# Kernel optimization log

Hardware: AMD Instinct MI355X
Metric: run time of the kernel (lower is better)

## Reference

```python
import jax, jax.numpy as jnp
import numpy as np

B, T, V, D, U = 256, 1024, 6, 64, 64  # batch, seq, vocab, embed dim, lstm units


def _lstm_dir(x_seq, mask_seq, Wk, Wr, b, reverse):
    # x_seq: [B,T,D], mask_seq: [B,T] bool. Keras gate order: i, f, g(cell), o.
    Bc, Tc, _ = x_seq.shape
    Uc = Wr.shape[0]
    if reverse:
        x_seq = x_seq[:, ::-1, :]
        mask_seq = mask_seq[:, ::-1]
    # precompute input projections for all timesteps (one big GEMM)
    xproj = jnp.einsum('btd,dg->tbg', x_seq, Wk) + b          # [T,B,4U]
    m = jnp.swapaxes(mask_seq, 0, 1)[..., None]               # [T,B,1]

    def step(carry, inp):
        h, c = carry
        xp, mt = inp
        z = xp + h @ Wr                                        # [B,4U]
        i, f, g, o = jnp.split(z, 4, axis=-1)
        i = jax.nn.sigmoid(i)
        f = jax.nn.sigmoid(f)
        g = jnp.tanh(g)
        o = jax.nn.sigmoid(o)
        c_new = f * c + i * g
        h_new = o * jnp.tanh(c_new)
        # masked steps carry state through and repeat previous output
        h = jnp.where(mt, h_new, h)
        c = jnp.where(mt, c_new, c)
        return (h, c), h

    h0 = jnp.zeros((Bc, Uc), x_seq.dtype)
    _, ys = jax.lax.scan(step, (h0, h0), (xproj, m))           # ys: [T,B,U]
    ys = jnp.swapaxes(ys, 0, 1)                                # [B,T,U]
    if reverse:
        ys = ys[:, ::-1, :]
    return ys


def reference(tokens, emb, Wk_f, Wr_f, b_f, Wk_b, Wr_b, b_b, Wd, bd):
    x = emb[tokens]                                            # [B,T,D]
    mask = jnp.any(x != 0, axis=-1)                            # Masking(0): all-zero feature vec -> masked
    y_f = _lstm_dir(x, mask, Wk_f, Wr_f, b_f, reverse=False)   # [B,T,U]
    y_b = _lstm_dir(x, mask, Wk_b, Wr_b, b_b, reverse=True)    # [B,T,U]
    y = jnp.concatenate([y_f, y_b], axis=-1)                   # [B,T,2U]
    last = y[:, -1, :]                                         # [B,2U]
    return last @ Wd + bd                                      # [B,1]


def setup_inputs() -> dict:
    key = jax.random.key(0)
    ks = jax.random.split(key, 8)
    return {
        'tokens': jax.random.randint(ks[0], (B, T), 0, V, dtype=jnp.int32),
        'emb': jax.random.normal(ks[1], (V, D), dtype=jnp.float32),
        'Wk_f': jax.random.normal(ks[2], (D, 4 * U), dtype=jnp.float32) * 0.05,
        'Wr_f': jax.random.normal(ks[3], (U, 4 * U), dtype=jnp.float32) * 0.05,
        'b_f': jnp.zeros((4 * U,), dtype=jnp.float32),
        'Wk_b': jax.random.normal(ks[4], (D, 4 * U), dtype=jnp.float32) * 0.05,
        'Wr_b': jax.random.normal(ks[5], (U, 4 * U), dtype=jnp.float32) * 0.05,
        'b_b': jnp.zeros((4 * U,), dtype=jnp.float32),
        'Wd': jax.random.normal(ks[6], (2 * U, 1), dtype=jnp.float32) * 0.05,
        'bd': jnp.zeros((1,), dtype=jnp.float32),
    }
```

## Files before the change

kernel.cpp:

```cpp
#include <hip/hip_runtime.h>


constexpr int kB = 256;
constexpr int kT = 1024;
constexpr int kV = 6;
constexpr int kD = 64;
constexpr int kU = 64;
constexpr int kG = 256;

#define LOG2E 1.44269504f

typedef _Float16 v2h __attribute__((ext_vector_type(2)));

template <int CTRL>
__device__ __forceinline__ float dppf(float x) {
    return __int_as_float(
        __builtin_amdgcn_mov_dpp(__float_as_int(x), CTRL, 0xF, 0xF, true));
}
constexpr int kBc0 = 0x00, kBc1 = 0x55, kBc2 = 0xAA, kBc3 = 0xFF;

__device__ __forceinline__ float fast_rcp(float x) { return __builtin_amdgcn_rcpf(x); }
__device__ __forceinline__ float exp2_f(float x)   { return __builtin_amdgcn_exp2f(x); }
__device__ __forceinline__ float sig_f(float z)  { return fast_rcp(1.0f + exp2_f(-LOG2E * z)); }
__device__ __forceinline__ float tanh_f(float z) { return 2.0f * fast_rcp(1.0f + exp2_f(-2.0f * LOG2E * z)) - 1.0f; }

__device__ __forceinline__ v2h as_v2h(float x) { return __builtin_bit_cast(v2h, x); }

__global__ __launch_bounds__(256)
__attribute__((amdgpu_waves_per_eu(1, 1)))
void bilstm_last_kernel(
    const int*   __restrict__ tokens,
    const float* __restrict__ emb,
    const float* __restrict__ Wk_f,
    const float* __restrict__ Wr_f,
    const float* __restrict__ b_f,
    const float* __restrict__ Wk_b,
    const float* __restrict__ b_b,
    const float* __restrict__ Wd,
    const float* __restrict__ bd,
    float*       __restrict__ out)
{
    __shared__ float s_emb[kV * kD];
    __shared__ float __align__(16) s_projP[kV * kG];
    __shared__ int   __align__(16) s_tok[kT];
    __shared__ _Float16 __align__(16) s_hh[2][kU];
    __shared__ float s_red[4];

    const int b   = blockIdx.x;
    const int tid = threadIdx.x;
    const int l   = tid & 63;
    const int wv  = tid >> 6;
    const int s   = l & 3;
    const int k   = l >> 2;
    const int u   = wv * 16 + k;
    const int col = s * kU + u;

    for (int i = tid; i < kV * kD; i += 256) s_emb[i] = emb[i];
    ((int4*)s_tok)[tid] = ((const int4*)(tokens + b * kT))[tid];
    if (tid < 2 * kU) ((_Float16*)s_hh)[tid] = (_Float16)0.f;
    __syncthreads();

    unsigned int mbv = 0;
#pragma unroll
    for (int v = 0; v < kV; ++v) {
        const unsigned long long bb = __ballot(s_emb[v * kD + l] != 0.0f);
        mbv |= (bb != 0ull) ? (1u << v) : 0u;
    }
    const unsigned int smb = __builtin_amdgcn_readfirstlane(mbv);

    const int tokL = __builtin_amdgcn_readfirstlane(s_tok[kT - 1]);

    float ab;
    {
        float afv[kV];
        const float bf = b_f[col];
#pragma unroll
        for (int v = 0; v < kV; ++v) afv[v] = bf;
        ab = b_b[col];
#pragma unroll 4
        for (int d = 0; d < kD; ++d) {
            const float wkf = Wk_f[d * kG + col];
            const float wkb = Wk_b[d * kG + col];
            afv[0] = fmaf(s_emb[0 * kD + d], wkf, afv[0]);
            afv[1] = fmaf(s_emb[1 * kD + d], wkf, afv[1]);
            afv[2] = fmaf(s_emb[2 * kD + d], wkf, afv[2]);
            afv[3] = fmaf(s_emb[3 * kD + d], wkf, afv[3]);
            afv[4] = fmaf(s_emb[4 * kD + d], wkf, afv[4]);
            afv[5] = fmaf(s_emb[5 * kD + d], wkf, afv[5]);
            ab     = fmaf(s_emb[tokL * kD + d], wkb, ab);
        }
#pragma unroll
        for (int v = 0; v < kV; ++v) s_projP[v * kG + tid] = afv[v];
    }

    const bool  isg    = (s == 2);
    const float aScale = isg ? -2.0f * LOG2E : -LOG2E;
    const float aMul   = isg ? 2.0f : 1.0f;
    const float aAdd   = isg ? -1.0f : 0.0f;

    float hb_val;
    {
        const float e = exp2_f(ab * aScale);
        const float r = fast_rcp(1.0f + e);
        const float a = fmaf(r, aMul, aAdd);
        const float ib = dppf<kBc0>(a);
        const float gb = dppf<kBc2>(a);
        const float ob = dppf<kBc3>(a);
        const float cb = ib * gb;
        const float hb = ob * tanh_f(cb);
        hb_val = ((smb >> tokL) & 1) ? hb : 0.0f;
    }

#define DECLW(p)                                                              \
    v2h wh_##p;                                                               \
    wh_##p.x = (_Float16)Wr_f[(2 * (p) + 0) * kG + col];                      \
    wh_##p.y = (_Float16)Wr_f[(2 * (p) + 1) * kG + col];
    DECLW(0)  DECLW(1)  DECLW(2)  DECLW(3)  DECLW(4)  DECLW(5)  DECLW(6)  DECLW(7)
    DECLW(8)  DECLW(9)  DECLW(10) DECLW(11) DECLW(12) DECLW(13) DECLW(14) DECLW(15)
    DECLW(16) DECLW(17) DECLW(18) DECLW(19) DECLW(20) DECLW(21) DECLW(22) DECLW(23)
    DECLW(24) DECLW(25) DECLW(26) DECLW(27) DECLW(28) DECLW(29) DECLW(30) DECLW(31)
#undef DECLW

    float c = 0.0f, hreg = 0.0f;

    int stok0 = __builtin_amdgcn_readfirstlane(s_tok[0]);
    float zcur = s_projP[stok0 * kG + tid];
    int mskc = (smb >> stok0) & 1;
    int stokA = __builtin_amdgcn_readfirstlane(s_tok[1]);

#define STEP(RP, WP, TT)                                                      \
    {                                                                         \
        const float4* hp = (const float4*)s_hh[RP];                           \
        const float4 hv0 = hp[0], hv1 = hp[1], hv2 = hp[2], hv3 = hp[3];      \
        const float4 hv4 = hp[4], hv5 = hp[5], hv6 = hp[6], hv7 = hp[7];      \
                          \
        const int   vtokB = s_tok[((TT) + 2) & (kT - 1)];                     \
        const float znext = s_projP[stokA * kG + tid];                        \
        const int   mskn  = (int)((smb >> stokA) & 1);                        \
        const v2h H0  = as_v2h(hv0.x), H1  = as_v2h(hv0.y);                   \
        const v2h H2  = as_v2h(hv0.z), H3  = as_v2h(hv0.w);                   \
        const v2h H4  = as_v2h(hv1.x), H5  = as_v2h(hv1.y);                   \
        const v2h H6  = as_v2h(hv1.z), H7  = as_v2h(hv1.w);                   \
        const v2h H8  = as_v2h(hv2.x), H9  = as_v2h(hv2.y);                   \
        const v2h H10 = as_v2h(hv2.z), H11 = as_v2h(hv2.w);                   \
        const v2h H12 = as_v2h(hv3.x), H13 = as_v2h(hv3.y);                   \
        const v2h H14 = as_v2h(hv3.z), H15 = as_v2h(hv3.w);                   \
        const v2h H16 = as_v2h(hv4.x), H17 = as_v2h(hv4.y);                   \
        const v2h H18 = as_v2h(hv4.z), H19 = as_v2h(hv4.w);                   \
        const v2h H20 = as_v2h(hv5.x), H21 = as_v2h(hv5.y);                   \
        const v2h H22 = as_v2h(hv5.z), H23 = as_v2h(hv5.w);                   \
        const v2h H24 = as_v2h(hv6.x), H25 = as_v2h(hv6.y);                   \
        const v2h H26 = as_v2h(hv6.z), H27 = as_v2h(hv6.w);                   \
        const v2h H28 = as_v2h(hv7.x), H29 = as_v2h(hv7.y);                   \
        const v2h H30 = as_v2h(hv7.z), H31 = as_v2h(hv7.w);                   \
                        \
        float pa = __builtin_amdgcn_fdot2(H0,  wh_0,  zcur, false);           \
        float pb = __builtin_amdgcn_fdot2(H1,  wh_1,  0.0f, false);           \
        float pc = __builtin_amdgcn_fdot2(H2,  wh_2,  0.0f, false);           \
        float pd = __builtin_amdgcn_fdot2(H3,  wh_3,  0.0f, false);           \
        pa = __builtin_amdgcn_fdot2(H4,  wh_4,  pa, false);                   \
        pb = __builtin_amdgcn_fdot2(H5,  wh_5,  pb, false);                   \
        pc = __builtin_amdgcn_fdot2(H6,  wh_6,  pc, false);                   \
        pd = __builtin_amdgcn_fdot2(H7,  wh_7,  pd, false);                   \
        pa = __builtin_amdgcn_fdot2(H8,  wh_8,  pa, false);                   \
        pb = __builtin_amdgcn_fdot2(H9,  wh_9,  pb, false);                   \
        pc = __builtin_amdgcn_fdot2(H10, wh_10, pc, false);                   \
        pd = __builtin_amdgcn_fdot2(H11, wh_11, pd, false);                   \
        pa = __builtin_amdgcn_fdot2(H12, wh_12, pa, false);                   \
        pb = __builtin_amdgcn_fdot2(H13, wh_13, pb, false);                   \
        pc = __builtin_amdgcn_fdot2(H14, wh_14, pc, false);                   \
        pd = __builtin_amdgcn_fdot2(H15, wh_15, pd, false);                   \
        pa = __builtin_amdgcn_fdot2(H16, wh_16, pa, false);                   \
        pb = __builtin_amdgcn_fdot2(H17, wh_17, pb, false);                   \
        pc = __builtin_amdgcn_fdot2(H18, wh_18, pc, false);                   \
        pd = __builtin_amdgcn_fdot2(H19, wh_19, pd, false);                   \
        pa = __builtin_amdgcn_fdot2(H20, wh_20, pa, false);                   \
        pb = __builtin_amdgcn_fdot2(H21, wh_21, pb, false);                   \
        pc = __builtin_amdgcn_fdot2(H22, wh_22, pc, false);                   \
        pd = __builtin_amdgcn_fdot2(H23, wh_23, pd, false);                   \
        pa = __builtin_amdgcn_fdot2(H24, wh_24, pa, false);                   \
        pb = __builtin_amdgcn_fdot2(H25, wh_25, pb, false);                   \
        pc = __builtin_amdgcn_fdot2(H26, wh_26, pc, false);                   \
        pd = __builtin_amdgcn_fdot2(H27, wh_27, pd, false);                   \
        pa = __builtin_amdgcn_fdot2(H28, wh_28, pa, false);                   \
        pb = __builtin_amdgcn_fdot2(H29, wh_29, pb, false);                   \
        pc = __builtin_amdgcn_fdot2(H30, wh_30, pc, false);                   \
        pd = __builtin_amdgcn_fdot2(H31, wh_31, pd, false);                   \
        const float z = (pa + pb) + (pc + pd);                                \
                                \
        const float e = exp2_f(z * aScale);                                   \
        const float r = fast_rcp(1.0f + e);                                   \
        const float a = fmaf(r, aMul, aAdd);                                  \
                  \
        const float ai = dppf<kBc0>(a);                                       \
        const float af = dppf<kBc1>(a);                                       \
        const float ag = dppf<kBc2>(a);                                       \
        const float ao = dppf<kBc3>(a);                                       \
        const float cn = fmaf(af, c, ai * ag);                                \
        const float hn = ao * tanh_f(cn);                                     \
        if (mskc) { c = cn; hreg = hn; }                  \
        if (s == 0) s_hh[WP][u] = (_Float16)hreg;                             \
        __syncthreads();                                                      \
        zcur = znext; mskc = mskn;                                            \
        stokA = __builtin_amdgcn_readfirstlane(vtokB);                        \
    }

#pragma unroll 1
    for (int t = 0; t < kT; t += 2) {
        STEP(0, 1, t)
        STEP(1, 0, t + 1)
    }
#undef STEP

    {
        float v = (s == 0) ? (hreg * Wd[u] + hb_val * Wd[kU + u]) : 0.0f;
#pragma unroll
        for (int off = 32; off > 0; off >>= 1) v += __shfl_down(v, off, 64);
        if (l == 0) s_red[wv] = v;
    }
    __syncthreads();
    if (tid == 0) out[b] = (s_red[0] + s_red[1]) + (s_red[2] + s_red[3]) + bd[0];
}

extern "C" void kernel_launch(void* const* d_in, const int* in_sizes, int n_in,
                              void* d_out, int out_size, void* d_ws, size_t ws_size,
                              hipStream_t stream) {
    const int*   tokens = (const int*)d_in[0];
    const float* emb    = (const float*)d_in[1];
    const float* Wk_f   = (const float*)d_in[2];
    const float* Wr_f   = (const float*)d_in[3];
    const float* b_f    = (const float*)d_in[4];
    const float* Wk_b   = (const float*)d_in[5];
    const float* b_b    = (const float*)d_in[7];
    const float* Wd     = (const float*)d_in[8];
    const float* bd     = (const float*)d_in[9];
    float* out = (float*)d_out;

    bilstm_last_kernel<<<kB, 256, 0, stream>>>(
        tokens, emb, Wk_f, Wr_f, b_f, Wk_b, b_b, Wd, bd, out);
}
```

Measured before the change: 349.5 us.

## Process two batch sequences per block to interleave independent recurrences

Each block now runs two batch rows' forward LSTM recurrences together, sharing the register-resident recurrent weights and one barrier per step. The two independent dot-product and gate chains can interleave, hiding the latency of the serial per-step chain and halving the number of barriers per sequence. In exchange the grid drops to 128 blocks, so only half the CUs are used, and register pressure rises.

```diff
diff --git a/kernel.cpp b/kernel.cpp
--- a/kernel.cpp
+++ b/kernel.cpp
@@ -42,11 +42,12 @@
 {
     __shared__ float s_emb[kV * kD];
     __shared__ float __align__(16) s_projP[kV * kG];
-    __shared__ int   __align__(16) s_tok[kT];
-    __shared__ _Float16 __align__(16) s_hh[2][kU];
-    __shared__ float s_red[4];
-
-    const int b   = blockIdx.x;
+    __shared__ int   __align__(16) s_tok[2][kT];
+    __shared__ _Float16 __align__(16) s_hh[2][2][kU];
+    __shared__ float s_red[2][4];
+
+    const int bP  = blockIdx.x * 2;
+    const int bQ  = bP + 1;
     const int tid = threadIdx.x;
     const int l   = tid & 63;
     const int wv  = tid >> 6;
@@ -56,8 +57,9 @@
     const int col = s * kU + u;
 
     for (int i = tid; i < kV * kD; i += 256) s_emb[i] = emb[i];
-    ((int4*)s_tok)[tid] = ((const int4*)(tokens + b * kT))[tid];
-    if (tid < 2 * kU) ((_Float16*)s_hh)[tid] = (_Float16)0.f;
+    ((int4*)s_tok[0])[tid] = ((const int4*)(tokens + bP * kT))[tid];
+    ((int4*)s_tok[1])[tid] = ((const int4*)(tokens + bQ * kT))[tid];
+    ((_Float16*)s_hh)[tid] = (_Float16)0.f;
     __syncthreads();
 
     unsigned int mbv = 0;
@@ -68,15 +70,16 @@
     }
     const unsigned int smb = __builtin_amdgcn_readfirstlane(mbv);
 
-    const int tokL = __builtin_amdgcn_readfirstlane(s_tok[kT - 1]);
-
-    float ab;
+    const int tokLP = __builtin_amdgcn_readfirstlane(s_tok[0][kT - 1]);
+    const int tokLQ = __builtin_amdgcn_readfirstlane(s_tok[1][kT - 1]);
+
+    float abP, abQ;
     {
         float afv[kV];
         const float bf = b_f[col];
 #pragma unroll
         for (int v = 0; v < kV; ++v) afv[v] = bf;
-        ab = b_b[col];
+        abP = b_b[col]; abQ = abP;
 #pragma unroll 4
         for (int d = 0; d < kD; ++d) {
             const float wkf = Wk_f[d * kG + col];
@@ -87,7 +90,8 @@
             afv[3] = fmaf(s_emb[3 * kD + d], wkf, afv[3]);
             afv[4] = fmaf(s_emb[4 * kD + d], wkf, afv[4]);
             afv[5] = fmaf(s_emb[5 * kD + d], wkf, afv[5]);
-            ab     = fmaf(s_emb[tokL * kD + d], wkb, ab);
+            abP    = fmaf(s_emb[tokLP * kD + d], wkb, abP);
+            abQ    = fmaf(s_emb[tokLQ * kD + d], wkb, abQ);
         }
 #pragma unroll
         for (int v = 0; v < kV; ++v) s_projP[v * kG + tid] = afv[v];
@@ -98,17 +102,20 @@
     const float aMul   = isg ? 2.0f : 1.0f;
     const float aAdd   = isg ? -1.0f : 0.0f;
 
-    float hb_val;
+    float hbP, hbQ;
     {
-        const float e = exp2_f(ab * aScale);
-        const float r = fast_rcp(1.0f + e);
-        const float a = fmaf(r, aMul, aAdd);
-        const float ib = dppf<kBc0>(a);
-        const float gb = dppf<kBc2>(a);
-        const float ob = dppf<kBc3>(a);
-        const float cb = ib * gb;
-        const float hb = ob * tanh_f(cb);
-        hb_val = ((smb >> tokL) & 1) ? hb : 0.0f;
+        const float eP = exp2_f(abP * aScale);
+        const float rP = fast_rcp(1.0f + eP);
+        const float aP = fmaf(rP, aMul, aAdd);
+        const float cbP = dppf<kBc0>(aP) * dppf<kBc2>(aP);
+        const float hP  = dppf<kBc3>(aP) * tanh_f(cbP);
+        hbP = ((smb >> tokLP) & 1) ? hP : 0.0f;
+        const float eQ = exp2_f(abQ * aScale);
+        const float rQ = fast_rcp(1.0f + eQ);
+        const float aQ = fmaf(rQ, aMul, aAdd);
+        const float cbQ = dppf<kBc0>(aQ) * dppf<kBc2>(aQ);
+        const float hQ  = dppf<kBc3>(aQ) * tanh_f(cbQ);
+        hbQ = ((smb >> tokLQ) & 1) ? hQ : 0.0f;
     }
 
 #define DECLW(p)                                                              \
@@ -121,88 +128,113 @@
     DECLW(24) DECLW(25) DECLW(26) DECLW(27) DECLW(28) DECLW(29) DECLW(30) DECLW(31)
 #undef DECLW
 
-    float c = 0.0f, hreg = 0.0f;
-
-    int stok0 = __builtin_amdgcn_readfirstlane(s_tok[0]);
-    float zcur = s_projP[stok0 * kG + tid];
-    int mskc = (smb >> stok0) & 1;
-    int stokA = __builtin_amdgcn_readfirstlane(s_tok[1]);
+    float cP = 0.0f, hregP = 0.0f;
+    float cQ = 0.0f, hregQ = 0.0f;
+
+    int stok0P = __builtin_amdgcn_readfirstlane(s_tok[0][0]);
+    int stok0Q = __builtin_amdgcn_readfirstlane(s_tok[1][0]);
+    float zcurP = s_projP[stok0P * kG + tid];
+    float zcurQ = s_projP[stok0Q * kG + tid];
+    int mskcP = (smb >> stok0P) & 1;
+    int mskcQ = (smb >> stok0Q) & 1;
+    int stokAP = __builtin_amdgcn_readfirstlane(s_tok[0][1]);
+    int stokAQ = __builtin_amdgcn_readfirstlane(s_tok[1][1]);
+
+#define HUNPACK(S, RP, Bi)                                                    \
+    const float4* hp##S = (const float4*)s_hh[RP][Bi];                        \
+    const float4 S##v0 = hp##S[0], S##v1 = hp##S[1];                          \
+    const float4 S##v2 = hp##S[2], S##v3 = hp##S[3];                          \
+    const float4 S##v4 = hp##S[4], S##v5 = hp##S[5];                          \
+    const float4 S##v6 = hp##S[6], S##v7 = hp##S[7];                          \
+    const v2h S##_0  = as_v2h(S##v0.x), S##_1  = as_v2h(S##v0.y);             \
+    const v2h S##_2  = as_v2h(S##v0.z), S##_3  = as_v2h(S##v0.w);             \
+    const v2h S##_4  = as_v2h(S##v1.x), S##_5  = as_v2h(S##v1.y);             \
+    const v2h S##_6  = as_v2h(S##v1.z), S##_7  = as_v2h(S##v1.w);             \
+    const v2h S##_8  = as_v2h(S##v2.x), S##_9  = as_v2h(S##v2.y);             \
+    const v2h S##_10 = as_v2h(S##v2.z), S##_11 = as_v2h(S##v2.w);             \
+    const v2h S##_12 = as_v2h(S##v3.x), S##_13 = as_v2h(S##v3.y);             \
+    const v2h S##_14 = as_v2h(S##v3.z), S##_15 = as_v2h(S##v3.w);             \
+    const v2h S##_16 = as_v2h(S##v4.x), S##_17 = as_v2h(S##v4.y);             \
+    const v2h S##_18 = as_v2h(S##v4.z), S##_19 = as_v2h(S##v4.w);             \
+    const v2h S##_20 = as_v2h(S##v5.x), S##_21 = as_v2h(S##v5.y);             \
+    const v2h S##_22 = as_v2h(S##v5.z), S##_23 = as_v2h(S##v5.w);             \
+    const v2h S##_24 = as_v2h(S##v6.x), S##_25 = as_v2h(S##v6.y);             \
+    const v2h S##_26 = as_v2h(S##v6.z), S##_27 = as_v2h(S##v6.w);             \
+    const v2h S##_28 = as_v2h(S##v7.x), S##_29 = as_v2h(S##v7.y);             \
+    const v2h S##_30 = as_v2h(S##v7.z), S##_31 = as_v2h(S##v7.w);
+
+#define DOT64(S, seed, zout)                                                  \
+    {                                                                         \
+        float pa = __builtin_amdgcn_fdot2(S##_0,  wh_0,  (seed), false);      \
+        float pb = __builtin_amdgcn_fdot2(S##_1,  wh_1,  0.0f, false);        \
+        float pc = __builtin_amdgcn_fdot2(S##_2,  wh_2,  0.0f, false);        \
+        float pd = __builtin_amdgcn_fdot2(S##_3,  wh_3,  0.0f, false);        \
+        pa = __builtin_amdgcn_fdot2(S##_4,  wh_4,  pa, false);                \
+        pb = __builtin_amdgcn_fdot2(S##_5,  wh_5,  pb, false);                \
+        pc = __builtin_amdgcn_fdot2(S##_6,  wh_6,  pc, false);                \
+        pd = __builtin_amdgcn_fdot2(S##_7,  wh_7,  pd, false);                \
+        pa = __builtin_amdgcn_fdot2(S##_8,  wh_8,  pa, false);                \
+        pb = __builtin_amdgcn_fdot2(S##_9,  wh_9,  pb, false);                \
+        pc = __builtin_amdgcn_fdot2(S##_10, wh_10, pc, false);                \
+        pd = __builtin_amdgcn_fdot2(S##_11, wh_11, pd, false);                \
+        pa = __builtin_amdgcn_fdot2(S##_12, wh_12, pa, false);                \
+        pb = __builtin_amdgcn_fdot2(S##_13, wh_13, pb, false);                \
+        pc = __builtin_amdgcn_fdot2(S##_14, wh_14, pc, false);                \
+        pd = __builtin_amdgcn_fdot2(S##_15, wh_15, pd, false);                \
+        pa = __builtin_amdgcn_fdot2(S##_16, wh_16, pa, false);                \
+        pb = __builtin_amdgcn_fdot2(S##_17, wh_17, pb, false);                \
+        pc = __builtin_amdgcn_fdot2(S##_18, wh_18, pc, false);                \
+        pd = __builtin_amdgcn_fdot2(S##_19, wh_19, pd, false);                \
+        pa = __builtin_amdgcn_fdot2(S##_20, wh_20, pa, false);                \
+        pb = __builtin_amdgcn_fdot2(S##_21, wh_21, pb, false);                \
+        pc = __builtin_amdgcn_fdot2(S##_22, wh_22, pc, false);                \
+        pd = __builtin_amdgcn_fdot2(S##_23, wh_23, pd, false);                \
+        pa = __builtin_amdgcn_fdot2(S##_24, wh_24, pa, false);                \
+        pb = __builtin_amdgcn_fdot2(S##_25, wh_25, pb, false);                \
+        pc = __builtin_amdgcn_fdot2(S##_26, wh_26, pc, false);                \
+        pd = __builtin_amdgcn_fdot2(S##_27, wh_27, pd, false);                \
+        pa = __builtin_amdgcn_fdot2(S##_28, wh_28, pa, false);                \
+        pb = __builtin_amdgcn_fdot2(S##_29, wh_29, pb, false);                \
+        pc = __builtin_amdgcn_fdot2(S##_30, wh_30, pc, false);                \
+        pd = __builtin_amdgcn_fdot2(S##_31, wh_31, pd, false);                \
+        zout = (pa + pb) + (pc + pd);                                         \
+    }
+
+#define GATEUPD(S, z, mskc, c, hreg, WP, Bi)                                  \
+    {                                                                         \
+        const float e_ = exp2_f((z) * aScale);                                \
+        const float r_ = fast_rcp(1.0f + e_);                                 \
+        const float a_ = fmaf(r_, aMul, aAdd);                                \
+        const float ai_ = dppf<kBc0>(a_);                                     \
+        const float af_ = dppf<kBc1>(a_);                                     \
+        const float ag_ = dppf<kBc2>(a_);                                     \
+        const float ao_ = dppf<kBc3>(a_);                                     \
+        const float cn_ = fmaf(af_, c, ai_ * ag_);                            \
+        const float hn_ = ao_ * tanh_f(cn_);                                  \
+        if (mskc) { c = cn_; hreg = hn_; }                \
+        if (s == 0) s_hh[WP][Bi][u] = (_Float16)hreg;                         \
+    }
 
 #define STEP(RP, WP, TT)                                                      \
     {                                                                         \
-        const float4* hp = (const float4*)s_hh[RP];                           \
-        const float4 hv0 = hp[0], hv1 = hp[1], hv2 = hp[2], hv3 = hp[3];      \
-        const float4 hv4 = hp[4], hv5 = hp[5], hv6 = hp[6], hv7 = hp[7];      \
-                          \
-        const int   vtokB = s_tok[((TT) + 2) & (kT - 1)];                     \
-        const float znext = s_projP[stokA * kG + tid];                        \
-        const int   mskn  = (int)((smb >> stokA) & 1);                        \
-        const v2h H0  = as_v2h(hv0.x), H1  = as_v2h(hv0.y);                   \
-        const v2h H2  = as_v2h(hv0.z), H3  = as_v2h(hv0.w);                   \
-        const v2h H4  = as_v2h(hv1.x), H5  = as_v2h(hv1.y);                   \
-        const v2h H6  = as_v2h(hv1.z), H7  = as_v2h(hv1.w);                   \
-        const v2h H8  = as_v2h(hv2.x), H9  = as_v2h(hv2.y);                   \
-        const v2h H10 = as_v2h(hv2.z), H11 = as_v2h(hv2.w);                   \
-        const v2h H12 = as_v2h(hv3.x), H13 = as_v2h(hv3.y);                   \
-        const v2h H14 = as_v2h(hv3.z), H15 = as_v2h(hv3.w);                   \
-        const v2h H16 = as_v2h(hv4.x), H17 = as_v2h(hv4.y);                   \
-        const v2h H18 = as_v2h(hv4.z), H19 = as_v2h(hv4.w);                   \
-        const v2h H20 = as_v2h(hv5.x), H21 = as_v2h(hv5.y);                   \
-        const v2h H22 = as_v2h(hv5.z), H23 = as_v2h(hv5.w);                   \
-        const v2h H24 = as_v2h(hv6.x), H25 = as_v2h(hv6.y);                   \
-        const v2h H26 = as_v2h(hv6.z), H27 = as_v2h(hv6.w);                   \
-        const v2h H28 = as_v2h(hv7.x), H29 = as_v2h(hv7.y);                   \
-        const v2h H30 = as_v2h(hv7.z), H31 = as_v2h(hv7.w);                   \
-                        \
-        float pa = __builtin_amdgcn_fdot2(H0,  wh_0,  zcur, false);           \
-        float pb = __builtin_amdgcn_fdot2(H1,  wh_1,  0.0f, false);           \
-        float pc = __builtin_amdgcn_fdot2(H2,  wh_2,  0.0f, false);           \
-        float pd = __builtin_amdgcn_fdot2(H3,  wh_3,  0.0f, false);           \
-        pa = __builtin_amdgcn_fdot2(H4,  wh_4,  pa, false);                   \
-        pb = __builtin_amdgcn_fdot2(H5,  wh_5,  pb, false);                   \
-        pc = __builtin_amdgcn_fdot2(H6,  wh_6,  pc, false);                   \
-        pd = __builtin_amdgcn_fdot2(H7,  wh_7,  pd, false);                   \
-        pa = __builtin_amdgcn_fdot2(H8,  wh_8,  pa, false);                   \
-        pb = __builtin_amdgcn_fdot2(H9,  wh_9,  pb, false);                   \
-        pc = __builtin_amdgcn_fdot2(H10, wh_10, pc, false);                   \
-        pd = __builtin_amdgcn_fdot2(H11, wh_11, pd, false);                   \
-        pa = __builtin_amdgcn_fdot2(H12, wh_12, pa, false);                   \
-        pb = __builtin_amdgcn_fdot2(H13, wh_13, pb, false);                   \
-        pc = __builtin_amdgcn_fdot2(H14, wh_14, pc, false);                   \
-        pd = __builtin_amdgcn_fdot2(H15, wh_15, pd, false);                   \
-        pa = __builtin_amdgcn_fdot2(H16, wh_16, pa, false);                   \
-        pb = __builtin_amdgcn_fdot2(H17, wh_17, pb, false);                   \
-        pc = __builtin_amdgcn_fdot2(H18, wh_18, pc, false);                   \
-        pd = __builtin_amdgcn_fdot2(H19, wh_19, pd, false);                   \
-        pa = __builtin_amdgcn_fdot2(H20, wh_20, pa, false);                   \
-        pb = __builtin_amdgcn_fdot2(H21, wh_21, pb, false);                   \
-        pc = __builtin_amdgcn_fdot2(H22, wh_22, pc, false);                   \
-        pd = __builtin_amdgcn_fdot2(H23, wh_23, pd, false);                   \
-        pa = __builtin_amdgcn_fdot2(H24, wh_24, pa, false);                   \
-        pb = __builtin_amdgcn_fdot2(H25, wh_25, pb, false);                   \
-        pc = __builtin_amdgcn_fdot2(H26, wh_26, pc, false);                   \
-        pd = __builtin_amdgcn_fdot2(H27, wh_27, pd, false);                   \
-        pa = __builtin_amdgcn_fdot2(H28, wh_28, pa, false);                   \
-        pb = __builtin_amdgcn_fdot2(H29, wh_29, pb, false);                   \
-        pc = __builtin_amdgcn_fdot2(H30, wh_30, pc, false);                   \
-        pd = __builtin_amdgcn_fdot2(H31, wh_31, pd, false);                   \
-        const float z = (pa + pb) + (pc + pd);                                \
-                                \
-        const float e = exp2_f(z * aScale);                                   \
-        const float r = fast_rcp(1.0f + e);                                   \
-        const float a = fmaf(r, aMul, aAdd);                                  \
-                  \
-        const float ai = dppf<kBc0>(a);                                       \
-        const float af = dppf<kBc1>(a);                                       \
-        const float ag = dppf<kBc2>(a);                                       \
-        const float ao = dppf<kBc3>(a);                                       \
-        const float cn = fmaf(af, c, ai * ag);                                \
-        const float hn = ao * tanh_f(cn);                                     \
-        if (mskc) { c = cn; hreg = hn; }                  \
-        if (s == 0) s_hh[WP][u] = (_Float16)hreg;                             \
+        HUNPACK(P, RP, 0)                                                     \
+        HUNPACK(Q, RP, 1)                                                     \
+        const int   vtokBP = s_tok[0][((TT) + 2) & (kT - 1)];                 \
+        const int   vtokBQ = s_tok[1][((TT) + 2) & (kT - 1)];                 \
+        const float znextP = s_projP[stokAP * kG + tid];                      \
+        const float znextQ = s_projP[stokAQ * kG + tid];                      \
+        const int   msknP  = (int)((smb >> stokAP) & 1);                      \
+        const int   msknQ  = (int)((smb >> stokAQ) & 1);                      \
+        float zP, zQ;                                                         \
+        DOT64(P, zcurP, zP)                                                   \
+        DOT64(Q, zcurQ, zQ)                                                   \
+        GATEUPD(P, zP, mskcP, cP, hregP, WP, 0)                               \
+        GATEUPD(Q, zQ, mskcQ, cQ, hregQ, WP, 1)                               \
         __syncthreads();                                                      \
-        zcur = znext; mskc = mskn;                                            \
-        stokA = __builtin_amdgcn_readfirstlane(vtokB);                        \
+        zcurP = znextP; mskcP = msknP;                                        \
+        zcurQ = znextQ; mskcQ = msknQ;                                        \
+        stokAP = __builtin_amdgcn_readfirstlane(vtokBP);                      \
+        stokAQ = __builtin_amdgcn_readfirstlane(vtokBQ);                      \
     }
 
 #pragma unroll 1
@@ -211,15 +243,25 @@
         STEP(1, 0, t + 1)
     }
 #undef STEP
+#undef GATEUPD
+#undef DOT64
+#undef HUNPACK
 
     {
-        float v = (s == 0) ? (hreg * Wd[u] + hb_val * Wd[kU + u]) : 0.0f;
+        float v = (s == 0) ? (hregP * Wd[u] + hbP * Wd[kU + u]) : 0.0f;
 #pragma unroll
         for (int off = 32; off > 0; off >>= 1) v += __shfl_down(v, off, 64);
-        if (l == 0) s_red[wv] = v;
+        if (l == 0) s_red[0][wv] = v;
+        float w = (s == 0) ? (hregQ * Wd[u] + hbQ * Wd[kU + u]) : 0.0f;
+#pragma unroll
+        for (int off = 32; off > 0; off >>= 1) w += __shfl_down(w, off, 64);
+        if (l == 0) s_red[1][wv] = w;
     }
     __syncthreads();
-    if (tid == 0) out[b] = (s_red[0] + s_red[1]) + (s_red[2] + s_red[3]) + bd[0];
+    if (tid == 0) {
+        out[bP] = (s_red[0][0] + s_red[0][1]) + (s_red[0][2] + s_red[0][3]) + bd[0];
+        out[bQ] = (s_red[1][0] + s_red[1][1]) + (s_red[1][2] + s_red[1][3]) + bd[0];
+    }
 }
 
 extern "C" void kernel_launch(void* const* d_in, const int* in_sizes, int n_in,
@@ -236,6 +278,6 @@
     const float* bd     = (const float*)d_in[9];
     float* out = (float*)d_out;
 
-    bilstm_last_kernel<<<kB, 256, 0, stream>>>(
+    bilstm_last_kernel<<<kB / 2, 256, 0, stream>>>(
         tokens, emb, Wk_f, Wr_f, b_f, Wk_b, b_b, Wd, bd, out);
 }
```

Measured after the change: 547.8 us. 56.8% more time.
